# Performance work log

Measured on AMD Instinct MI355X. Metric: run time of the kernel, lower is better.

Reference implementation:

```python
import jax, jax.numpy as jnp
import numpy as np

D_HEAD = 64

def setup_inputs() -> dict:
    key = jax.random.key(0)
    k1, k2, k3, k4, k5 = jax.random.split(key, 5)
    B, S, D, H, Dh = 2, 2048, 1024, 16, D_HEAD
    std = 0.02
    return {
        "residual": jax.random.normal(k1, (B, S, D), dtype=jnp.float32),
        "W_Q": jax.random.normal(k2, (H, Dh, D), dtype=jnp.float32) * std,
        "W_K": jax.random.normal(k3, (H, Dh, D), dtype=jnp.float32) * std,
        "W_V": jax.random.normal(k4, (H, Dh, D), dtype=jnp.float32) * std,
        "W_O": jax.random.normal(k5, (H, Dh, D), dtype=jnp.float32) * std,
    }

def reference(residual, W_Q, W_K, W_V, W_O):
    # residual: [b, s, d]; W_*: [h, e, d] with e = d_head
    S = residual.shape[1]
    q = jnp.einsum('bsd,hed->bshe', residual, W_Q)
    k = jnp.einsum('bsd,hed->bshe', residual, W_K)
    v = jnp.einsum('bsd,hed->bshe', residual, W_V)
    scale = 1.0 / jnp.sqrt(jnp.asarray(D_HEAD, dtype=residual.dtype))
    scores = jnp.einsum('bqhe,bkhe->bhqk', q, k) * scale  # [b,h,s,s]
    causal = jnp.tril(jnp.ones((S, S), dtype=bool))
    scores = jnp.where(causal, scores, -jnp.inf)
    pattern = jax.nn.softmax(scores, axis=-1)
    attn_out = jnp.einsum('bhqk,bkhe->bqhe', pattern, v)
    out = jnp.einsum('bqhe,hed->bqd', attn_out, W_O)
    return out
```

## Files before the change

### kernel.cpp

```cpp
#include <hip/hip_runtime.h>
#include <math.h>

typedef unsigned short bf16;
typedef unsigned long long u64;
typedef __attribute__((ext_vector_type(8))) short short8;
typedef __attribute__((ext_vector_type(4))) float f32x4;

#define S_LEN 2048
#define NH    16
#define DH    64
#define DM    1024
#define BATCH 2

__device__ __forceinline__ bf16 f2bf(float f) {
    unsigned u = __float_as_uint(f);
    u += 0x7fffu + ((u >> 16) & 1u);
    return (bf16)(u >> 16);
}

__device__ __forceinline__ unsigned pack2(float a, float b) {
    unsigned ua = __float_as_uint(a) + 0x8000u;
    unsigned ub = __float_as_uint(b) + 0x8000u;
    return (ua >> 16) | (ub & 0xFFFF0000u);
}

__device__ __forceinline__ u64 pack4(f32x4 v) {
    return (u64)pack2(v[0], v[1]) | ((u64)pack2(v[2], v[3]) << 32);
}

__device__ __forceinline__ float fast_exp2(float x) {
#if __has_builtin(__builtin_amdgcn_exp2f)
    return __builtin_amdgcn_exp2f(x);
#else
    return exp2f(x);
#endif
}

__device__ __forceinline__ void gload_lds16(const void* g, void* s) {
    __builtin_amdgcn_global_load_lds(
        (const __attribute__((address_space(1))) unsigned int*)g,
        (__attribute__((address_space(3))) unsigned int*)s, 16, 0, 0);
}

#define QSCALE 0.18033688011112042f

__global__ __launch_bounds__(256) void convert_kernel(
    const float* __restrict__ X,  const float* __restrict__ WQ,
    const float* __restrict__ WK, const float* __restrict__ WV,
    const float* __restrict__ WO,
    bf16* __restrict__ Xb, bf16* __restrict__ WQb, bf16* __restrict__ WKb,
    bf16* __restrict__ WVb, bf16* __restrict__ WOt)
{
    __shared__ float T[64][65];
    const int blk = blockIdx.x;
    if (blk < 7168) {
        const int t = blk * 256 + threadIdx.x;
        if (t < 1048576) {
            float4 v = ((const float4*)X)[t];
            u64 pk = (u64)f2bf(v.x) | ((u64)f2bf(v.y) << 16)
                   | ((u64)f2bf(v.z) << 32) | ((u64)f2bf(v.w) << 48);
            *(u64*)(Xb + 4 * (size_t)t) = pk;
        } else if (t < 1310720) {
            int i = t - 1048576;
            float4 v = ((const float4*)WQ)[i];
            u64 pk = (u64)f2bf(v.x * QSCALE) | ((u64)f2bf(v.y * QSCALE) << 16)
                   | ((u64)f2bf(v.z * QSCALE) << 32) | ((u64)f2bf(v.w * QSCALE) << 48);
            *(u64*)(WQb + 4 * (size_t)i) = pk;
        } else if (t < 1572864) {
            int i = t - 1310720;
            float4 v = ((const float4*)WK)[i];
            u64 pk = (u64)f2bf(v.x) | ((u64)f2bf(v.y) << 16)
                   | ((u64)f2bf(v.z) << 32) | ((u64)f2bf(v.w) << 48);
            *(u64*)(WKb + 4 * (size_t)i) = pk;
        } else {
            int i = t - 1572864;
            float4 v = ((const float4*)WV)[i];
            u64 pk = (u64)f2bf(v.x) | ((u64)f2bf(v.y) << 16)
                   | ((u64)f2bf(v.z) << 32) | ((u64)f2bf(v.w) << 48);
            *(u64*)(WVb + 4 * (size_t)i) = pk;
        }
    } else {
        const int tile = blk - 7168;
        const int he0 = (tile & 15) * 64, d0 = (tile >> 4) * 64;
        const int tid = threadIdx.x;
        const int row = tid >> 2, c0 = (tid & 3) * 16;
        #pragma unroll
        for (int u = 0; u < 4; ++u) {
            float4 v = *(const float4*)(WO + (size_t)(he0 + row) * DM + d0 + c0 + u * 4);
            T[row][c0 + u * 4 + 0] = v.x;
            T[row][c0 + u * 4 + 1] = v.y;
            T[row][c0 + u * 4 + 2] = v.z;
            T[row][c0 + u * 4 + 3] = v.w;
        }
        __syncthreads();
        bf16 tmp[16];
        #pragma unroll
        for (int j = 0; j < 16; ++j) tmp[j] = f2bf(T[c0 + j][row]);
        *(short8*)(WOt + (size_t)(d0 + row) * DM + he0 + c0)     = *(short8*)&tmp[0];
        *(short8*)(WOt + (size_t)(d0 + row) * DM + he0 + c0 + 8) = *(short8*)&tmp[8];
    }
}

__global__ __launch_bounds__(256) void proj_kernel(
    const bf16* __restrict__ Xb, const bf16* __restrict__ WQb,
    const bf16* __restrict__ WKb, const bf16* __restrict__ WVb,
    bf16* __restrict__ qbuf, bf16* __restrict__ kbuf, bf16* __restrict__ vt)
{
    __shared__ char lds[65536];

    const int id = blockIdx.x;
    const int tid = threadIdx.x, wave = tid >> 6, lane = tid & 63;
    const int tx = lane & 15, quad = lane >> 4;
    const int wm = (wave >> 1) * 64, wn = (wave & 1) * 64;

    int mode, am0, bn0, bb = 0;
    const bf16 *Aop, *Bop;
    if (id < 512) {
        mode = id & 1;
        int rem = id >> 1;
        bn0 = (rem & 31) * 128;
        am0 = (rem >> 5) * 128;
        Aop = (mode ? WKb : WQb) + (size_t)am0 * DM;
        Bop = Xb + (size_t)bn0 * DM;
    } else {
        mode = 2;
        int rem = id - 512;
        bb = rem & 1;
        rem >>= 1;
        bn0 = (rem & 7) * 128;
        am0 = (rem >> 3) * 128;
        Aop = Xb + ((size_t)bb * S_LEN + am0) * DM;
        Bop = WVb + (size_t)bn0 * DM;
    }

    f32x4 acc[4][4] = {};

    {
        char* As = lds;
        char* Bs = lds + 16384;
        #pragma unroll
        for (int r = 0; r < 4; ++r) {
            int slot = r * 256 + tid;
            int row = slot >> 3, g = slot & 7, gl = g ^ (row & 7);
            gload_lds16(Aop + (size_t)row * DM + gl * 8, As + r * 4096 + wave * 1024);
            gload_lds16(Bop + (size_t)row * DM + gl * 8, Bs + r * 4096 + wave * 1024);
        }
    }

    for (int kt = 0; kt < 16; ++kt) {
        char* As = lds + (kt & 1) * 32768;
        char* Bs = As + 16384;
        __syncthreads();

        if (kt < 15) {
            char* An = lds + ((kt + 1) & 1) * 32768;
            char* Bn = An + 16384;
            const int k0 = (kt + 1) * 64;
            #pragma unroll
            for (int r = 0; r < 4; ++r) {
                int slot = r * 256 + tid;
                int row = slot >> 3, g = slot & 7, gl = g ^ (row & 7);
                gload_lds16(Aop + (size_t)row * DM + k0 + gl * 8,
                            An + r * 4096 + wave * 1024);
                gload_lds16(Bop + (size_t)row * DM + k0 + gl * 8,
                            Bn + r * 4096 + wave * 1024);
            }
        }

        #pragma unroll
        for (int ks = 0; ks < 2; ++ks) {
            const int swz = ((ks * 4 + quad) ^ (tx & 7)) * 16;
            short8 af[4], bfr[4];
            #pragma unroll
            for (int mt = 0; mt < 4; ++mt)
                af[mt] = *(const short8*)(As + (wm + mt * 16 + tx) * 128 + swz);
            #pragma unroll
            for (int nt = 0; nt < 4; ++nt)
                bfr[nt] = *(const short8*)(Bs + (wn + nt * 16 + tx) * 128 + swz);
            #pragma unroll
            for (int mt = 0; mt < 4; ++mt)
                #pragma unroll
                for (int nt = 0; nt < 4; ++nt)
                    acc[mt][nt] = __builtin_amdgcn_mfma_f32_16x16x32_bf16(
                        af[mt], bfr[nt], acc[mt][nt], 0, 0, 0);
        }
    }

    if (mode < 2) {
        bf16* outb = mode ? kbuf : qbuf;
        #pragma unroll
        for (int mt = 0; mt < 4; ++mt)
            #pragma unroll
            for (int nt = 0; nt < 4; ++nt) {
                int heG  = am0 + wm + mt * 16 + quad * 4;
                int tokG = bn0 + wn + nt * 16 + tx;
                int b = tokG >> 11, s = tokG & 2047;
                int h = heG >> 6, e0 = heG & 63;
                *(u64*)(outb + ((size_t)(b * NH + h) * S_LEN + s) * DH + e0) =
                    pack4(acc[mt][nt]);
            }
    } else {
        #pragma unroll
        for (int mt = 0; mt < 4; ++mt)
            #pragma unroll
            for (int nt = 0; nt < 4; ++nt) {
                int sG  = am0 + wm + mt * 16 + quad * 4;
                int heG = bn0 + wn + nt * 16 + tx;
                *(u64*)(vt + ((size_t)bb * DM + heG) * S_LEN + sG) =
                    pack4(acc[mt][nt]);
            }
    }
}

__global__ __launch_bounds__(256) void flash_kernel(
    const bf16* __restrict__ qbuf, const bf16* __restrict__ kbuf,
    const bf16* __restrict__ vtb, bf16* __restrict__ attn)
{
    __shared__ char lds[49152];
    char* Pts = lds + 32768;

    const int i  = blockIdx.x;
    const int bh = i & 31;
    const int j  = i >> 5;
    const int qb = (i < 256) ? (15 - j) : (j - 8);
    const int tid = threadIdx.x, wave = tid >> 6, lane = tid & 63;
    const int tx = lane & 15, quad = lane >> 4;
    const int sw = tx & 7;

    const bf16* Qg = qbuf + (size_t)bh * S_LEN * DH + (size_t)qb * 128 * DH;
    const bf16* Kg = kbuf + (size_t)bh * S_LEN * DH;
    const bf16* Vg = vtb  + (size_t)bh * DH * S_LEN;

    short8 bq[2][2];
    #pragma unroll
    for (int g = 0; g < 2; ++g)
        #pragma unroll
        for (int es = 0; es < 2; ++es)
            bq[g][es] = *(const short8*)(Qg + (size_t)(wave * 32 + g * 16 + tx) * DH +
                                         (es * 4 + quad) * 8);

    f32x4 oacc[2][4] = {};
    float l_part[2] = {0.0f, 0.0f};

    const int kmax  = 2 * qb + 1;
    const int wdiag = 2 * qb + (wave >> 1);
    const int qg0   = qb * 128 + wave * 32 + tx;

    char* Pw = Pts + wave * 4096;

    {
        char* Kb = lds;
        char* Vb = lds + 8192;
        #pragma unroll
        for (int r = 0; r < 2; ++r) {
            int slot = r * 256 + tid;
            int row = slot >> 3, g = slot & 7, gl = g ^ (row & 7);
            gload_lds16(Kg + (size_t)row * DH + gl * 8, Kb + r * 4096 + wave * 1024);
            gload_lds16(Vg + (size_t)row * S_LEN + gl * 8, Vb + r * 4096 + wave * 1024);
        }
    }

    for (int kt64 = 0; kt64 <= kmax; ++kt64) {
        char* Kc = lds + (kt64 & 1) * 16384;
        char* Vc = Kc + 8192;
        __syncthreads();

        if (kt64 < kmax) {
            char* Kn = lds + ((kt64 + 1) & 1) * 16384;
            char* Vn = Kn + 8192;
            #pragma unroll
            for (int r = 0; r < 2; ++r) {
                int slot = r * 256 + tid;
                int row = slot >> 3, g = slot & 7, gl = g ^ (row & 7);
                gload_lds16(Kg + ((size_t)(kt64 + 1) * 64 + row) * DH + gl * 8,
                            Kn + r * 4096 + wave * 1024);
                gload_lds16(Vg + (size_t)row * S_LEN + (kt64 + 1) * 64 + gl * 8,
                            Vn + r * 4096 + wave * 1024);
            }
        }

        if (kt64 <= wdiag) {
            f32x4 st[2][4] = {};
            #pragma unroll
            for (int es = 0; es < 2; ++es) {
                #pragma unroll
                for (int kt = 0; kt < 4; ++kt) {
                    short8 ak = *(const short8*)(Kc + (kt * 16 + tx) * 128 +
                                                 (((es * 4 + quad) ^ sw) * 16));
                    #pragma unroll
                    for (int g = 0; g < 2; ++g)
                        st[g][kt] = __builtin_amdgcn_mfma_f32_16x16x32_bf16(
                            ak, bq[g][es], st[g][kt], 0, 0, 0);
                }
            }

            if (kt64 == wdiag) {
                #pragma unroll
                for (int g = 0; g < 2; ++g)
                    #pragma unroll
                    for (int kt = 0; kt < 4; ++kt)
                        #pragma unroll
                        for (int r = 0; r < 4; ++r)
                            if (kt64 * 64 + kt * 16 + quad * 4 + r > qg0 + g * 16)
                                st[g][kt][r] = -1e30f;
            }

            #pragma unroll
            for (int g = 0; g < 2; ++g) {
                float rs = 0.0f;
                #pragma unroll
                for (int kt = 0; kt < 4; ++kt) {
                    #pragma unroll
                    for (int r = 0; r < 4; ++r) {
                        float p = fast_exp2(st[g][kt][r]);
                        st[g][kt][r] = p;
                        rs += p;
                    }
                    unsigned lo = pack2(st[g][kt][0], st[g][kt][1]);
                    unsigned hi = pack2(st[g][kt][2], st[g][kt][3]);
                    int kg = kt * 2 + (quad >> 1);
                    *(uint2*)(Pw + (g * 16 + tx) * 128 + ((kg ^ sw) * 16) +
                              (quad & 1) * 8) = make_uint2(lo, hi);
                }
                l_part[g] += rs;
            }
            asm volatile("s_waitcnt lgkmcnt(0)" ::: "memory");

            #pragma unroll
            for (int ks = 0; ks < 2; ++ks) {
                const int swz = ((ks * 4 + quad) ^ sw) * 16;
                short8 bp[2];
                #pragma unroll
                for (int g = 0; g < 2; ++g)
                    bp[g] = *(const short8*)(Pw + (g * 16 + tx) * 128 + swz);
                #pragma unroll
                for (int et = 0; et < 4; ++et) {
                    short8 av = *(const short8*)(Vc + (et * 16 + tx) * 128 + swz);
                    #pragma unroll
                    for (int g = 0; g < 2; ++g)
                        oacc[g][et] = __builtin_amdgcn_mfma_f32_16x16x32_bf16(
                            av, bp[g], oacc[g][et], 0, 0, 0);
                }
            }
        }
    }

    const int b = bh >> 4, h = bh & 15;
    #pragma unroll
    for (int g = 0; g < 2; ++g) {
        float l = l_part[g];
        l += __shfl_xor(l, 16);
        l += __shfl_xor(l, 32);
        float inv = 1.0f / l;
        #pragma unroll
        for (int et = 0; et < 4; ++et) {
            unsigned lo = pack2(oacc[g][et][0] * inv, oacc[g][et][1] * inv);
            unsigned hi = pack2(oacc[g][et][2] * inv, oacc[g][et][3] * inv);
            int eg = et * 2 + (quad >> 1);
            *(uint2*)(Pw + (g * 16 + tx) * 128 + ((eg ^ sw) * 16) +
                      (quad & 1) * 8) = make_uint2(lo, hi);
        }
    }
    asm volatile("s_waitcnt lgkmcnt(0)" ::: "memory");

    #pragma unroll
    for (int g = 0; g < 2; ++g) {
        const int s = qb * 128 + wave * 32 + g * 16 + tx;
        bf16* op = attn + ((size_t)b * S_LEN + s) * DM + h * DH;
        #pragma unroll
        for (int c2 = 0; c2 < 2; ++c2) {
            int c = quad + c2 * 4;
            short8 v = *(const short8*)(Pw + (g * 16 + tx) * 128 + ((c ^ sw) * 16));
            *(short8*)(op + c * 8) = v;
        }
    }
}

__global__ __launch_bounds__(256) void out_proj_kernel(
    const bf16* __restrict__ A, const bf16* __restrict__ Bt,
    float* __restrict__ out)
{
    __shared__ char lds[49152];

    const int m0 = blockIdx.x * 128, n0 = blockIdx.y * 64;
    const int tid = threadIdx.x, wave = tid >> 6, lane = tid & 63;
    const int tx = lane & 15, quad = lane >> 4;
    const int wm = wave * 32;

    f32x4 acc[2][4] = {};

    {
        char* As = lds;
        char* Bs = lds + 16384;
        #pragma unroll
        for (int r = 0; r < 4; ++r) {
            int slot = r * 256 + tid;
            int row = slot >> 3, g = slot & 7, gl = g ^ (row & 7);
            gload_lds16(A + (size_t)(m0 + row) * DM + gl * 8,
                        As + r * 4096 + wave * 1024);
        }
        #pragma unroll
        for (int r = 0; r < 2; ++r) {
            int slot = r * 256 + tid;
            int row = slot >> 3, g = slot & 7, gl = g ^ (row & 7);
            gload_lds16(Bt + (size_t)(n0 + row) * DM + gl * 8,
                        Bs + r * 4096 + wave * 1024);
        }
    }

    for (int kt = 0; kt < 16; ++kt) {
        char* As = lds + (kt & 1) * 24576;
        char* Bs = As + 16384;
        __syncthreads();

        if (kt < 15) {
            char* An = lds + ((kt + 1) & 1) * 24576;
            char* Bn = An + 16384;
            const int k0 = (kt + 1) * 64;
            #pragma unroll
            for (int r = 0; r < 4; ++r) {
                int slot = r * 256 + tid;
                int row = slot >> 3, g = slot & 7, gl = g ^ (row & 7);
                gload_lds16(A + (size_t)(m0 + row) * DM + k0 + gl * 8,
                            An + r * 4096 + wave * 1024);
            }
            #pragma unroll
            for (int r = 0; r < 2; ++r) {
                int slot = r * 256 + tid;
                int row = slot >> 3, g = slot & 7, gl = g ^ (row & 7);
                gload_lds16(Bt + (size_t)(n0 + row) * DM + k0 + gl * 8,
                            Bn + r * 4096 + wave * 1024);
            }
        }

        #pragma unroll
        for (int ks = 0; ks < 2; ++ks) {
            const int swz = ((ks * 4 + quad) ^ (tx & 7)) * 16;
            short8 af[2], bfr[4];
            #pragma unroll
            for (int mt = 0; mt < 2; ++mt)
                af[mt] = *(const short8*)(As + (wm + mt * 16 + tx) * 128 + swz);
            #pragma unroll
            for (int nt = 0; nt < 4; ++nt)
                bfr[nt] = *(const short8*)(Bs + (nt * 16 + tx) * 128 + swz);
            #pragma unroll
            for (int mt = 0; mt < 2; ++mt)
                #pragma unroll
                for (int nt = 0; nt < 4; ++nt)
                    acc[mt][nt] = __builtin_amdgcn_mfma_f32_16x16x32_bf16(
                        af[mt], bfr[nt], acc[mt][nt], 0, 0, 0);
        }
    }

    #pragma unroll
    for (int mt = 0; mt < 2; ++mt)
        #pragma unroll
        for (int nt = 0; nt < 4; ++nt)
            #pragma unroll
            for (int r = 0; r < 4; ++r) {
                int mG = m0 + wm + mt * 16 + quad * 4 + r;
                int nG = n0 + nt * 16 + tx;
                out[(size_t)mG * DM + nG] = acc[mt][nt][r];
            }
}

extern "C" void kernel_launch(void* const* d_in, const int* in_sizes, int n_in,
                              void* d_out, int out_size, void* d_ws, size_t ws_size,
                              hipStream_t stream) {
    const float* X  = (const float*)d_in[0];
    const float* WQ = (const float*)d_in[1];
    const float* WK = (const float*)d_in[2];
    const float* WV = (const float*)d_in[3];
    const float* WO = (const float*)d_in[4];
    float* out = (float*)d_out;

    char* ws = (char*)d_ws;
    bf16* Xb   = (bf16*)(ws);
    bf16* WQb  = (bf16*)(ws + (8u  << 20));
    bf16* WKb  = (bf16*)(ws + (10u << 20));
    bf16* WVb  = (bf16*)(ws + (12u << 20));
    bf16* WOt  = (bf16*)(ws + (14u << 20));
    bf16* qbuf = (bf16*)(ws + (16u << 20));
    bf16* kbuf = (bf16*)(ws + (24u << 20));
    bf16* vt   = (bf16*)(ws + (32u << 20));
    bf16* attn = (bf16*)(ws + (40u << 20));

    convert_kernel<<<7424, 256, 0, stream>>>(X, WQ, WK, WV, WO,
                                             Xb, WQb, WKb, WVb, WOt);
    proj_kernel<<<768, 256, 0, stream>>>(Xb, WQb, WKb, WVb, qbuf, kbuf, vt);
    flash_kernel<<<512, 256, 0, stream>>>(qbuf, kbuf, vt, attn);
    out_proj_kernel<<<dim3(32, 16), 256, 0, stream>>>(attn, WOt, out);
}
```

Measured before the change: 171.1 us.

## Keep softmax probabilities in registers and use 16x16x16 MFMA for PV

The probability tile no longer round-trips through LDS. The exp'd scores are packed into bf16x4 registers that match the accumulator layout of the 16x16x16 bf16 MFMA, and the PV product is computed directly with that smaller-K instruction. This removes LDS writes, a waitcnt, and re-reads of P per tile, and shrinks shared memory from 48KB to 32KB, which may raise occupancy. In exchange it issues twice as many MFMA instructions at half the K depth, and V is read in narrower 8-byte chunks. The epilogue staging buffer is moved into the K/V region.

```diff
diff --git a/kernel.cpp b/kernel.cpp
--- a/kernel.cpp
+++ b/kernel.cpp
@@ -4,6 +4,7 @@
 typedef unsigned short bf16;
 typedef unsigned long long u64;
 typedef __attribute__((ext_vector_type(8))) short short8;
+typedef __attribute__((ext_vector_type(4))) short s16x4;
 typedef __attribute__((ext_vector_type(4))) float f32x4;
 
 #define S_LEN 2048
@@ -26,6 +27,12 @@
 
 __device__ __forceinline__ u64 pack4(f32x4 v) {
     return (u64)pack2(v[0], v[1]) | ((u64)pack2(v[2], v[3]) << 32);
+}
+
+__device__ __forceinline__ s16x4 pack4s(f32x4 v) {
+    union { uint2 u; s16x4 s; } cv;
+    cv.u = make_uint2(pack2(v[0], v[1]), pack2(v[2], v[3]));
+    return cv.s;
 }
 
 __device__ __forceinline__ float fast_exp2(float x) {
@@ -216,8 +223,7 @@
     const bf16* __restrict__ qbuf, const bf16* __restrict__ kbuf,
     const bf16* __restrict__ vtb, bf16* __restrict__ attn)
 {
-    __shared__ char lds[49152];
-    char* Pts = lds + 32768;
+    __shared__ char lds[32768];
 
     const int i  = blockIdx.x;
     const int bh = i & 31;
@@ -246,18 +252,13 @@
     const int wdiag = 2 * qb + (wave >> 1);
     const int qg0   = qb * 128 + wave * 32 + tx;
 
-    char* Pw = Pts + wave * 4096;
-
-    {
-        char* Kb = lds;
-        char* Vb = lds + 8192;
-        #pragma unroll
-        for (int r = 0; r < 2; ++r) {
-            int slot = r * 256 + tid;
-            int row = slot >> 3, g = slot & 7, gl = g ^ (row & 7);
-            gload_lds16(Kg + (size_t)row * DH + gl * 8, Kb + r * 4096 + wave * 1024);
-            gload_lds16(Vg + (size_t)row * S_LEN + gl * 8, Vb + r * 4096 + wave * 1024);
-        }
+    #pragma unroll
+    for (int r = 0; r < 2; ++r) {
+        int slot = r * 256 + tid;
+        int row = slot >> 3, g = slot & 7, gl = g ^ (row & 7);
+        gload_lds16(Kg + (size_t)row * DH + gl * 8, lds + r * 4096 + wave * 1024);
+        gload_lds16(Vg + (size_t)row * S_LEN + gl * 8,
+                    lds + 8192 + r * 4096 + wave * 1024);
     }
 
     for (int kt64 = 0; kt64 <= kmax; ++kt64) {
@@ -305,6 +306,7 @@
                                 st[g][kt][r] = -1e30f;
             }
 
+            s16x4 pb[2][4];
             #pragma unroll
             for (int g = 0; g < 2; ++g) {
                 float rs = 0.0f;
@@ -316,36 +318,28 @@
                         st[g][kt][r] = p;
                         rs += p;
                     }
-                    unsigned lo = pack2(st[g][kt][0], st[g][kt][1]);
-                    unsigned hi = pack2(st[g][kt][2], st[g][kt][3]);
-                    int kg = kt * 2 + (quad >> 1);
-                    *(uint2*)(Pw + (g * 16 + tx) * 128 + ((kg ^ sw) * 16) +
-                              (quad & 1) * 8) = make_uint2(lo, hi);
+                    pb[g][kt] = pack4s(st[g][kt]);
                 }
                 l_part[g] += rs;
             }
-            asm volatile("s_waitcnt lgkmcnt(0)" ::: "memory");
-
-            #pragma unroll
-            for (int ks = 0; ks < 2; ++ks) {
-                const int swz = ((ks * 4 + quad) ^ sw) * 16;
-                short8 bp[2];
-                #pragma unroll
-                for (int g = 0; g < 2; ++g)
-                    bp[g] = *(const short8*)(Pw + (g * 16 + tx) * 128 + swz);
+
+            #pragma unroll
+            for (int kt = 0; kt < 4; ++kt) {
                 #pragma unroll
                 for (int et = 0; et < 4; ++et) {
-                    short8 av = *(const short8*)(Vc + (et * 16 + tx) * 128 + swz);
+                    s16x4 av = *(const s16x4*)(Vc + (et * 16 + tx) * 128 +
+                                 (((kt * 2 + (quad >> 1)) ^ sw) * 16) + (quad & 1) * 8);
                     #pragma unroll
                     for (int g = 0; g < 2; ++g)
-                        oacc[g][et] = __builtin_amdgcn_mfma_f32_16x16x32_bf16(
-                            av, bp[g], oacc[g][et], 0, 0, 0);
+                        oacc[g][et] = __builtin_amdgcn_mfma_f32_16x16x16bf16_1k(
+                            av, pb[g][kt], oacc[g][et], 0, 0, 0);
                 }
             }
         }
     }
 
     const int b = bh >> 4, h = bh & 15;
+    char* Pw = lds + wave * 4096;
     #pragma unroll
     for (int g = 0; g < 2; ++g) {
         float l = l_part[g];
```

New measurement: 169.8 us. About the same (-0.8%).
